# Optimization experiments

Measured on AMD Instinct MI355X. Metric: run time of the kernel, lower is better.

## Reference

```python
import jax, jax.numpy as jnp
import numpy as np

NUM_HEADS = 12
EPS = 1e-12  # torch F.normalize clamp_min eps


def _l2norm(t):
    return t / jnp.clip(jnp.linalg.norm(t, axis=-1, keepdims=True), EPS)


def setup_inputs() -> dict:
    key = jax.random.key(0)
    ks = jax.random.split(key, 6)
    B, N, C = 8, 4096, 768
    Nc, Nb, F = 1, 512, 16
    s = 0.02
    return {
        "x": jax.random.normal(ks[0], (B, N, C), jnp.float32),
        "bank": jax.random.normal(ks[1], (Nc, Nb, F), jnp.float32),
        "Wq": jax.random.normal(ks[2], (C, C), jnp.float32) * s,
        "Wkv": jax.random.normal(ks[3], (F, 2 * C), jnp.float32) * s,
        "Wlin": jax.random.normal(ks[4], (C, C), jnp.float32) * s,
        "b_lin": jnp.zeros((C,), jnp.float32),
        "prelu_a": jnp.asarray(0.25, jnp.float32),
        "temperature": jnp.ones((NUM_HEADS, 1, 1), jnp.float32),
    }


def reference(x, bank, Wq, Wkv, Wlin, b_lin, prelu_a, temperature):
    B, N, C = x.shape
    Nc, Nb, _ = bank.shape
    H = NUM_HEADS
    d = C // H
    # q: (B, H, N, d), L2-normalized along d
    q = _l2norm((x @ Wq).reshape(B, N, H, d).transpose(0, 2, 1, 3))
    # kv from (detached) bank: (2, Nc, H, Nb, d)
    kv = (bank @ Wkv).reshape(Nc, Nb, 2, H, d).transpose(2, 0, 3, 1, 4)
    k = _l2norm(kv[0])
    v = kv[1]
    # cosine attention with per-head learned temperature: (B, Nc, H, N, Nb)
    attn = jnp.einsum('bhnd,chmd->bchnm', q, k) * temperature
    attn = jax.nn.softmax(attn, axis=-1)
    # (dropout is identity in eval mode)
    out = jnp.einsum('bchnm,chmd->bchnd', attn, v)  # (B, Nc, H, N, d)
    out = out.reshape(B * Nc, H, N, d).transpose(0, 2, 1, 3).reshape(B, N, C)
    out = out @ Wlin + b_lin
    # PReLU with a single shared parameter
    return jnp.where(out >= 0, out, prelu_a * out)
```

## Files before the change

kernel.cpp:

```cpp
#include <hip/hip_runtime.h>
#include <cstdint>
#include <cstddef>

typedef unsigned short u16;
typedef __attribute__((ext_vector_type(8))) __bf16 bf16x8;
typedef __attribute__((ext_vector_type(4))) float f32x4;

#define MFMA(a, b, c) __builtin_amdgcn_mfma_f32_16x16x32_bf16(a, b, c, 0, 0, 0)

__device__ __forceinline__ u16 f2bf(float f) {
  union { float f; uint32_t u; } x; x.f = f;
  uint32_t r = x.u + 0x7fffu + ((x.u >> 16) & 1u);
  return (u16)(r >> 16);
}

__device__ __forceinline__ void gld16(const u16* g, u16* l) {
  __builtin_amdgcn_global_load_lds(
      (const __attribute__((address_space(1))) void*)g,
      (__attribute__((address_space(3))) void*)l, 16, 0, 0);
}

__global__ void cvt_f32_bf16(const float* __restrict__ src, u16* __restrict__ dst, int n4) {
  int i = blockIdx.x * blockDim.x + threadIdx.x;
  int stride = gridDim.x * blockDim.x;
  for (; i < n4; i += stride) {
    float4 v = ((const float4*)src)[i];
    ushort4 o;
    o.x = f2bf(v.x); o.y = f2bf(v.y); o.z = f2bf(v.z); o.w = f2bf(v.w);
    ((ushort4*)dst)[i] = o;
  }
}

__global__ void transpose_cvt(const float* __restrict__ src, u16* __restrict__ dst, int R, int C) {
  __shared__ float tile[32][33];
  int bx = blockIdx.x * 32, by = blockIdx.y * 32;
  int tx = threadIdx.x, ty = threadIdx.y;
  #pragma unroll
  for (int i = ty; i < 32; i += 8)
    tile[i][tx] = src[(size_t)(by + i) * C + bx + tx];
  __syncthreads();
  #pragma unroll
  for (int i = ty; i < 32; i += 8)
    dst[(size_t)(bx + i) * R + by + tx] = f2bf(tile[tx][i]);
}

__global__ void kv_prep(const float* __restrict__ bank, const float* __restrict__ Wkv,
                        const float* __restrict__ temp, u16* __restrict__ K, u16* __restrict__ VT) {
  int m = blockIdx.x & 511, h = blockIdx.x >> 9;
  int j = threadIdx.x;
  const float* br = bank + m * 16;
  float kj = 0.f, vj = 0.f;
  #pragma unroll
  for (int f = 0; f < 16; ++f) {
    float bv = br[f];
    kj = fmaf(bv, Wkv[f * 1536 + h * 64 + j], kj);
    vj = fmaf(bv, Wkv[f * 1536 + 768 + h * 64 + j], vj);
  }
  float ss = kj * kj;
  #pragma unroll
  for (int o = 32; o; o >>= 1) ss += __shfl_xor(ss, o);
  float rn = rsqrtf(fmaxf(ss, 1e-24f));
  K[((size_t)h * 512 + m) * 64 + j] = f2bf(kj * rn * temp[h] * 1.4426950408889634f);
  VT[((size_t)h * 64 + j) * 512 + m] = f2bf(vj);
}

template <int MODE>
__global__ __launch_bounds__(256, 3) void gemm_bt(
    const u16* __restrict__ A, const u16* __restrict__ BT, void* __restrict__ Cout,
    int M, int N, int K, const float* __restrict__ bias, const float* __restrict__ prelu) {
  __shared__ u16 sA[128 * 32];
  __shared__ u16 sB[128 * 32];
  const int ntiles = N >> 7;
  const int m0 = (blockIdx.x / ntiles) << 7;
  const int n0 = (blockIdx.x % ntiles) << 7;
  const int tid = threadIdx.x;
  const int w = tid >> 6, lane = tid & 63;
  const int wm = (w >> 1) << 6, wn = (w & 1) << 6;
  const int srow = lane >> 2, scol = (lane & 3) << 3;
  const u16* ga = A + (size_t)(m0 + (w << 5) + srow) * K + scol;
  const u16* gb = BT + (size_t)(n0 + (w << 5) + srow) * K + scol;
  u16* la = sA + (w << 5) * 32;
  u16* lb = sB + (w << 5) * 32;
  const int fr = lane & 15, fq = (lane >> 4) << 3;
  f32x4 acc[4][4] = {};

  for (int k0 = 0; k0 < K; k0 += 32) {
    __syncthreads();
    gld16(ga + k0, la);
    gld16(ga + k0 + (size_t)16 * K, la + 16 * 32);
    gld16(gb + k0, lb);
    gld16(gb + k0 + (size_t)16 * K, lb + 16 * 32);
    __syncthreads();
    bf16x8 af[4], bfr[4];
    #pragma unroll
    for (int t = 0; t < 4; ++t) {
      af[t] = *(const bf16x8*)(sA + (wm + t * 16 + fr) * 32 + fq);
      bfr[t] = *(const bf16x8*)(sB + (wn + t * 16 + fr) * 32 + fq);
    }
    #pragma unroll
    for (int i = 0; i < 4; ++i)
      #pragma unroll
      for (int j = 0; j < 4; ++j)
        acc[i][j] = MFMA(af[i], bfr[j], acc[i][j]);
  }

  const int q = lane >> 4;
  float a = (MODE == 1) ? prelu[0] : 0.f;
  #pragma unroll
  for (int tm = 0; tm < 4; ++tm)
    #pragma unroll
    for (int tn = 0; tn < 4; ++tn) {
      int col = n0 + wn + tn * 16 + fr;
      float bv = (MODE == 1) ? bias[col] : 0.f;
      #pragma unroll
      for (int r = 0; r < 4; ++r) {
        int row = m0 + wm + tm * 16 + q * 4 + r;
        float v = acc[tm][tn][r];
        if (MODE == 1) {
          v += bv;
          v = v >= 0.f ? v : v * a;
          ((float*)Cout)[(size_t)row * N + col] = v;
        } else {
          ((u16*)Cout)[(size_t)row * N + col] = f2bf(v);
        }
      }
    }
}

__global__ __launch_bounds__(256, 2) void attn_kern(
    const u16* __restrict__ Q, const u16* __restrict__ Kb,
    const u16* __restrict__ Vt, u16* __restrict__ O) {
  __shared__ __align__(16) u16 sK[2][64 * 72];
  __shared__ __align__(16) u16 sV[2][64 * 72];
  __shared__ __align__(16) u16 pb_s[4][64 * 40];

  const int qb = blockIdx.x & 127;
  const int h = blockIdx.x >> 7;
  const int tid = threadIdx.x, w = tid >> 6, lane = tid & 63;
  const int fr = lane & 15, quad = lane >> 4;
  const int rowbase = qb * 256 + (w << 6);

  bf16x8 qa[4][2];
  #pragma unroll
  for (int g = 0; g < 4; ++g) {
    const u16* qp = Q + (size_t)(rowbase + g * 16 + fr) * 768 + h * 64 + (quad << 3);
    qa[g][0] = *(const bf16x8*)qp;
    qa[g][1] = *(const bf16x8*)(qp + 32);
    float ss = 0.f;
    #pragma unroll
    for (int j = 0; j < 8; ++j) {
      float f0 = (float)qa[g][0][j], f1 = (float)qa[g][1][j];
      ss += f0 * f0 + f1 * f1;
    }
    ss += __shfl_xor(ss, 16);
    ss += __shfl_xor(ss, 32);
    float rn = rsqrtf(fmaxf(ss, 1e-24f));
    #pragma unroll
    for (int j = 0; j < 8; ++j) {
      qa[g][0][j] = (__bf16)((float)qa[g][0][j] * rn);
      qa[g][1][j] = (__bf16)((float)qa[g][1][j] * rn);
    }
  }

  const u16* kg = Kb + (size_t)h * 512 * 64;
  const u16* vg = Vt + (size_t)h * 64 * 512;
  int4 kreg[2], vreg[2];
  auto load_chunk = [&](int c) {
    #pragma unroll
    for (int r = 0; r < 2; ++r) {
      int u = r * 256 + tid;
      kreg[r] = *(const int4*)(kg + (size_t)(c * 64 + (u >> 3)) * 64 + (u & 7) * 8);
      vreg[r] = *(const int4*)(vg + (size_t)(u >> 3) * 512 + c * 64 + (u & 7) * 8);
    }
  };
  auto store_chunk = [&](int buf) {
    #pragma unroll
    for (int r = 0; r < 2; ++r) {
      int u = r * 256 + tid;
      *(int4*)(sK[buf] + (u >> 3) * 72 + (u & 7) * 8) = kreg[r];
      *(int4*)(sV[buf] + (u >> 3) * 72 + (u & 7) * 8) = vreg[r];
    }
  };

  load_chunk(0);
  store_chunk(0);
  load_chunk(1);
  __syncthreads();

  f32x4 oa[4][4] = {};
  float ls[4] = {0.f, 0.f, 0.f, 0.f};
  u16* pw = pb_s[w];

  for (int c = 0; c < 8; ++c) {
    const int cb = c & 1;
    if (c < 7) store_chunk((c + 1) & 1);
    if (c < 6) load_chunk(c + 2);

    f32x4 s[4][4];
    #pragma unroll
    for (int mt = 0; mt < 4; ++mt) {
      const u16* kp = sK[cb] + (mt * 16 + fr) * 72 + (quad << 3);
      bf16x8 ak0 = *(const bf16x8*)kp;
      bf16x8 ak1 = *(const bf16x8*)(kp + 32);
      #pragma unroll
      for (int g = 0; g < 4; ++g) {
        f32x4 z = {0.f, 0.f, 0.f, 0.f};
        z = MFMA(ak0, qa[g][0], z);
        z = MFMA(ak1, qa[g][1], z);
        s[g][mt] = z;
      }
    }
    #pragma unroll
    for (int g = 0; g < 4; ++g)
      #pragma unroll
      for (int mt = 0; mt < 4; ++mt)
        #pragma unroll
        for (int r = 0; r < 4; ++r) {
          float p = __builtin_amdgcn_exp2f(s[g][mt][r]);
          ls[g] += p;
          s[g][mt][r] = p;
        }
    #pragma unroll
    for (int ks = 0; ks < 2; ++ks) {
      #pragma unroll
      for (int g = 0; g < 4; ++g)
        #pragma unroll
        for (int i = 0; i < 2; ++i) {
          f32x4 v = s[g][ks * 2 + i];
          uint32_t lo = (uint32_t)f2bf(v[0]) | ((uint32_t)f2bf(v[1]) << 16);
          uint32_t hi = (uint32_t)f2bf(v[2]) | ((uint32_t)f2bf(v[3]) << 16);
          uint2 pk = {lo, hi};
          *(uint2*)(pw + (g * 16 + fr) * 40 + i * 16 + (quad << 2)) = pk;
        }
      bf16x8 va[4], pbf[4];
      #pragma unroll
      for (int t = 0; t < 4; ++t)
        va[t] = *(const bf16x8*)(sV[cb] + (t * 16 + fr) * 72 + ks * 32 + (quad << 3));
      #pragma unroll
      for (int g = 0; g < 4; ++g)
        pbf[g] = *(const bf16x8*)(pw + (g * 16 + fr) * 40 + (quad << 3));
      #pragma unroll
      for (int g = 0; g < 4; ++g)
        #pragma unroll
        for (int t = 0; t < 4; ++t)
          oa[g][t] = MFMA(va[t], pbf[g], oa[g][t]);
    }
    __syncthreads();
  }

  #pragma unroll
  for (int g = 0; g < 4; ++g) {
    float l = ls[g];
    l += __shfl_xor(l, 16);
    l += __shfl_xor(l, 32);
    float rl = __builtin_amdgcn_rcpf(l);
    u16* op = O + (size_t)(rowbase + g * 16 + fr) * 768 + h * 64 + (quad << 2);
    #pragma unroll
    for (int t = 0; t < 4; ++t) {
      ushort4 pk;
      pk.x = f2bf(oa[g][t][0] * rl);
      pk.y = f2bf(oa[g][t][1] * rl);
      pk.z = f2bf(oa[g][t][2] * rl);
      pk.w = f2bf(oa[g][t][3] * rl);
      *(ushort4*)(op + t * 16) = pk;
    }
  }
}

extern "C" void kernel_launch(void* const* d_in, const int* in_sizes, int n_in,
                              void* d_out, int out_size, void* d_ws, size_t ws_size,
                              hipStream_t stream) {
  const float* x      = (const float*)d_in[0];
  const float* bank   = (const float*)d_in[1];
  const float* Wq     = (const float*)d_in[2];
  const float* Wkv    = (const float*)d_in[3];
  const float* Wlin   = (const float*)d_in[4];
  const float* b_lin  = (const float*)d_in[5];
  const float* prelu  = (const float*)d_in[6];
  const float* temp   = (const float*)d_in[7];
  float* out = (float*)d_out;

  char* ws = (char*)d_ws;
  const size_t NELEM = 25165824;
  u16* qbuf  = (u16*)ws;
  u16* xbuf  = (u16*)(ws + 50331648);
  u16* obuf  = xbuf;
  u16* wqt   = (u16*)(ws + 100663296);
  u16* wlt   = wqt + 589824;
  u16* kbuf  = wlt + 589824;
  u16* vtbuf = kbuf + 393216;

  cvt_f32_bf16<<<4096, 256, 0, stream>>>(x, xbuf, (int)(NELEM / 4));
  transpose_cvt<<<dim3(24, 24), dim3(32, 8), 0, stream>>>(Wq, wqt, 768, 768);
  transpose_cvt<<<dim3(24, 24), dim3(32, 8), 0, stream>>>(Wlin, wlt, 768, 768);
  kv_prep<<<6144, 64, 0, stream>>>(bank, Wkv, temp, kbuf, vtbuf);
  gemm_bt<0><<<1536, 256, 0, stream>>>(xbuf, wqt, qbuf, 32768, 768, 768, nullptr, nullptr);
  attn_kern<<<1536, 256, 0, stream>>>(qbuf, kbuf, vtbuf, obuf);
  gemm_bt<1><<<1536, 256, 0, stream>>>(obuf, wlt, out, 32768, 768, 768, b_lin, prelu);
}
```

Baseline: 436.0 us.

## Keep softmax probabilities in registers by permuting V fragment loads, drop LDS P buffer

The attention kernel no longer round-trips the exponentiated scores through a per-wave LDS buffer. It builds the PV MFMA operand straight from the QK accumulator registers, and loads V from shared memory in a matching permuted k-order (two 8-byte reads per fragment). S is computed in two halves so fewer score registers are live at once. Occupancy is raised to 3 blocks per CU. This removes LDS writes and reads and the implied wave-local dependency, but the more register-constrained launch bound may cause spills.

```diff
diff --git a/kernel.cpp b/kernel.cpp
--- a/kernel.cpp
+++ b/kernel.cpp
@@ -127,12 +127,11 @@
     }
 }
 
-__global__ __launch_bounds__(256, 2) void attn_kern(
+__global__ __launch_bounds__(256, 3) void attn_kern(
     const u16* __restrict__ Q, const u16* __restrict__ Kb,
     const u16* __restrict__ Vt, u16* __restrict__ O) {
   __shared__ __align__(16) u16 sK[2][64 * 72];
   __shared__ __align__(16) u16 sV[2][64 * 72];
-  __shared__ __align__(16) u16 pb_s[4][64 * 40];
 
   const int qb = blockIdx.x & 127;
   const int h = blockIdx.x >> 7;
@@ -189,61 +188,50 @@
 
   f32x4 oa[4][4] = {};
   float ls[4] = {0.f, 0.f, 0.f, 0.f};
-  u16* pw = pb_s[w];
 
   for (int c = 0; c < 8; ++c) {
     const int cb = c & 1;
     if (c < 7) store_chunk((c + 1) & 1);
     if (c < 6) load_chunk(c + 2);
 
-    f32x4 s[4][4];
-    #pragma unroll
-    for (int mt = 0; mt < 4; ++mt) {
-      const u16* kp = sK[cb] + (mt * 16 + fr) * 72 + (quad << 3);
-      bf16x8 ak0 = *(const bf16x8*)kp;
-      bf16x8 ak1 = *(const bf16x8*)(kp + 32);
-      #pragma unroll
-      for (int g = 0; g < 4; ++g) {
-        f32x4 z = {0.f, 0.f, 0.f, 0.f};
-        z = MFMA(ak0, qa[g][0], z);
-        z = MFMA(ak1, qa[g][1], z);
-        s[g][mt] = z;
+    #pragma unroll
+    for (int ks = 0; ks < 2; ++ks) {
+      f32x4 s[4][2];
+      #pragma unroll
+      for (int half = 0; half < 2; ++half) {
+        const int mt = ks * 2 + half;
+        const u16* kp = sK[cb] + (mt * 16 + fr) * 72 + (quad << 3);
+        bf16x8 ak0 = *(const bf16x8*)kp;
+        bf16x8 ak1 = *(const bf16x8*)(kp + 32);
+        #pragma unroll
+        for (int g = 0; g < 4; ++g) {
+          f32x4 z = {0.f, 0.f, 0.f, 0.f};
+          z = MFMA(ak0, qa[g][0], z);
+          z = MFMA(ak1, qa[g][1], z);
+          s[g][half] = z;
+        }
       }
-    }
-    #pragma unroll
-    for (int g = 0; g < 4; ++g)
-      #pragma unroll
-      for (int mt = 0; mt < 4; ++mt)
-        #pragma unroll
-        for (int r = 0; r < 4; ++r) {
-          float p = __builtin_amdgcn_exp2f(s[g][mt][r]);
-          ls[g] += p;
-          s[g][mt][r] = p;
-        }
-    #pragma unroll
-    for (int ks = 0; ks < 2; ++ks) {
+      bf16x8 pbf[4];
       #pragma unroll
       for (int g = 0; g < 4; ++g)
         #pragma unroll
-        for (int i = 0; i < 2; ++i) {
-          f32x4 v = s[g][ks * 2 + i];
-          uint32_t lo = (uint32_t)f2bf(v[0]) | ((uint32_t)f2bf(v[1]) << 16);
-          uint32_t hi = (uint32_t)f2bf(v[2]) | ((uint32_t)f2bf(v[3]) << 16);
-          uint2 pk = {lo, hi};
-          *(uint2*)(pw + (g * 16 + fr) * 40 + i * 16 + (quad << 2)) = pk;
-        }
-      bf16x8 va[4], pbf[4];
-      #pragma unroll
-      for (int t = 0; t < 4; ++t)
-        va[t] = *(const bf16x8*)(sV[cb] + (t * 16 + fr) * 72 + ks * 32 + (quad << 3));
-      #pragma unroll
-      for (int g = 0; g < 4; ++g)
-        pbf[g] = *(const bf16x8*)(pw + (g * 16 + fr) * 40 + (quad << 3));
-      #pragma unroll
-      for (int g = 0; g < 4; ++g)
+        for (int half = 0; half < 2; ++half)
+          #pragma unroll
+          for (int r = 0; r < 4; ++r) {
+            float p = __builtin_amdgcn_exp2f(s[g][half][r]);
+            ls[g] += p;
+            pbf[g][half * 4 + r] = (__bf16)p;
+          }
+      #pragma unroll
+      for (int t = 0; t < 4; ++t) {
+        const u16* vp = sV[cb] + (t * 16 + fr) * 72 + ks * 32 + (quad << 2);
+        bf16x8 va;
+        *(uint2*)&va = *(const uint2*)vp;
+        *((uint2*)&va + 1) = *(const uint2*)(vp + 16);
         #pragma unroll
-        for (int t = 0; t < 4; ++t)
-          oa[g][t] = MFMA(va[t], pbf[g], oa[g][t]);
+        for (int g = 0; g < 4; ++g)
+          oa[g][t] = MFMA(va, pbf[g], oa[g][t]);
+      }
     }
     __syncthreads();
   }
```

Result: slower. 576.7 us (+32.3%).
